# Kernel optimization log

Hardware: AMD Instinct MI355X
Metric: run time of the kernel (lower is better)

## Reference

```python
import jax, jax.numpy as jnp
import numpy as np

B, S, E = 2, 2048, 1024
H = 16
D = E // H  # head_dim = 64
SCALE = D ** -0.5


def _rope_cos_sin(seq_len, dim, dtype=jnp.float32):
    inv_freq = 1.0 / (10000.0 ** (jnp.arange(0, dim, 2, dtype=jnp.float32) / dim))
    pos = jnp.arange(seq_len, dtype=jnp.float32)
    freqs = pos[:, None] * inv_freq[None, :]  # [S, D/2]
    return jnp.cos(freqs).astype(dtype), jnp.sin(freqs).astype(dtype)


def _apply_rope(x, cos, sin):
    # x: [B, H, S, D]; interleaved complex rotation on (even, odd) pairs
    x2 = x.reshape(*x.shape[:-1], D // 2, 2)
    xr, xi = x2[..., 0], x2[..., 1]
    c = cos[None, None, :, :]
    s = sin[None, None, :, :]
    out_r = xr * c - xi * s
    out_i = xr * s + xi * c
    return jnp.stack([out_r, out_i], axis=-1).reshape(x.shape)


def setup_inputs() -> dict:
    key = jax.random.key(0)
    k1, k2, k3, k4, k5 = jax.random.split(key, 5)
    query = jax.random.normal(k1, (B, S, E), dtype=jnp.float32)
    key_t = jax.random.normal(k2, (B, S, E), dtype=jnp.float32)
    value = jax.random.normal(k3, (B, S, E), dtype=jnp.float32)
    w_qkv = jax.random.normal(k4, (3 * E, E), dtype=jnp.float32) * 0.02
    w_out = jax.random.normal(k5, (E, E), dtype=jnp.float32) * 0.02
    return {"query": query, "key": key_t, "value": value,
            "w_qkv": w_qkv, "w_out": w_out}


def reference(query, key, value, w_qkv, w_out):
    # Fused QKV projection from query only (matches original module)
    qkv = jnp.einsum('bse,fe->bsf', query, w_qkv)  # [B, S, 3E]
    q, k, v = jnp.split(qkv, 3, axis=-1)
    to_heads = lambda t: t.reshape(B, S, H, D).transpose(0, 2, 1, 3)  # [B,H,S,D]
    q, k, v = to_heads(q), to_heads(k), to_heads(v)

    cos, sin = _rope_cos_sin(S, D, q.dtype)
    q = _apply_rope(q, cos, sin)
    k = _apply_rope(k, cos, sin)

    # Standard scaled dot-product attention (eval mode, no mask, no dropout)
    attn = jnp.einsum('bhsd,bhtd->bhst', q, k) * SCALE
    attn = jax.nn.softmax(attn.astype(jnp.float32), axis=-1).astype(q.dtype)
    ctx = jnp.einsum('bhst,bhtd->bhsd', attn, v)  # [B,H,S,D]

    out = ctx.transpose(0, 2, 1, 3).reshape(B, S, E)
    return jnp.einsum('bse,fe->bsf', out, w_out)
```

## Files before the change

kernel.cpp:

```cpp
#include <hip/hip_runtime.h>
#include <math.h>

typedef __attribute__((ext_vector_type(8))) __bf16 bf16x8;
typedef __attribute__((ext_vector_type(4))) __bf16 bf16x4;
typedef __attribute__((ext_vector_type(4))) float f32x4;

constexpr int kBATCH = 2;
constexpr int kS = 2048;
constexpr int kE = 1024;
constexpr int kH = 16;
constexpr int kD = 64;
constexpr float kScale = 0.125f;
constexpr float kQScale = 0.125f * 1.44269504088896340736f;

__device__ inline void gl2lds16(const void* g, void* l) {
    __builtin_amdgcn_global_load_lds((const __attribute__((address_space(1))) void*)g,
                                     (__attribute__((address_space(3))) void*)l, 16, 0, 0);
}

__global__ __launch_bounds__(256) void cvt2_kernel(const float* __restrict__ a, __bf16* __restrict__ oa, int na,
                                                   const float* __restrict__ b, __bf16* __restrict__ ob,
                                                   float2* __restrict__ tab) {
    if (blockIdx.x >= 7168) {
        int e = (blockIdx.x - 7168) * 1024 + threadIdx.x * 4;
#pragma unroll
        for (int j = 0; j < 4; ++j) {
            int ee = e + j;
            int s = ee >> 5, i = ee & 31;
            float inv = expf(-(float)i * (9.210340371976184f / 32.0f));
            float ang = (float)s * inv;
            tab[ee] = make_float2(cosf(ang), sinf(ang));
        }
        return;
    }
    int idx = (blockIdx.x * 256 + threadIdx.x) * 4;
    const float* src;
    __bf16* dst;
    if (idx < na) { src = a + idx; dst = oa + idx; }
    else          { src = b + (idx - na); dst = ob + (idx - na); }
    float4 f = *(const float4*)src;
    bf16x4 r;
    r[0] = (__bf16)f.x; r[1] = (__bf16)f.y; r[2] = (__bf16)f.z; r[3] = (__bf16)f.w;
    *(bf16x4*)dst = r;
}

__global__ __launch_bounds__(256) void gemm_qkv_kernel(const __bf16* __restrict__ A,
                                                       const __bf16* __restrict__ W,
                                                       __bf16* __restrict__ vraw,
                                                       __bf16* __restrict__ qd,
                                                       __bf16* __restrict__ kd,
                                                       const float2* __restrict__ tab) {
    constexpr int kK = 1024;
    __shared__ __bf16 As[128 * 64] __attribute__((aligned(16)));
    __shared__ __bf16 Bs[128 * 64] __attribute__((aligned(16)));

    const int tid  = threadIdx.x;
    const int lane = tid & 63;
    const int quad = lane >> 4;
    const int l16  = lane & 15;
    const int rx   = l16 & 7;
    const int wave = tid >> 6;
    const int wm   = (wave >> 1) * 64;
    const int wn   = (wave & 1) * 64;
    const int m0   = blockIdx.y * 128;
    const int n0   = blockIdx.x * 128;

    const int srow8  = lane >> 3;
    const int schunk = ((lane & 7) ^ srow8) * 8;

    f32x4 zero = {0.f, 0.f, 0.f, 0.f};
    f32x4 acc[4][4];
#pragma unroll
    for (int i = 0; i < 4; ++i)
#pragma unroll
        for (int j = 0; j < 4; ++j) acc[i][j] = zero;

    for (int kt = 0; kt < kK; kt += 64) {
        __syncthreads();
#pragma unroll
        for (int i = 0; i < 4; ++i) {
            int rbase = wave * 32 + i * 8;
            gl2lds16(A + (size_t)(m0 + rbase + srow8) * kK + kt + schunk, &As[rbase * 64]);
            gl2lds16(W + (size_t)(n0 + rbase + srow8) * kK + kt + schunk, &Bs[rbase * 64]);
        }
        __syncthreads();

#pragma unroll
        for (int kk = 0; kk < 2; ++kk) {
            bf16x8 af[4], bf[4];
#pragma unroll
            for (int mi = 0; mi < 4; ++mi)
                af[mi] = *(const bf16x8*)(&As[(wm + mi * 16 + l16) * 64 + (((kk * 4 + quad) ^ rx)) * 8]);
#pragma unroll
            for (int ni = 0; ni < 4; ++ni)
                bf[ni] = *(const bf16x8*)(&Bs[(wn + ni * 16 + l16) * 64 + (((kk * 4 + quad) ^ rx)) * 8]);
#pragma unroll
            for (int mi = 0; mi < 4; ++mi)
#pragma unroll
                for (int ni = 0; ni < 4; ++ni)
                    acc[mi][ni] = __builtin_amdgcn_mfma_f32_16x16x32_bf16(af[mi], bf[ni], acc[mi][ni], 0, 0, 0);
        }
    }

    const int col0 = n0 + wn;
    const int reg  = col0 >> 10;
    const int h    = (col0 >> 6) & 15;

    if (reg == 2) {
#pragma unroll
        for (int mi = 0; mi < 4; ++mi)
#pragma unroll
            for (int ni = 0; ni < 4; ++ni)
#pragma unroll
                for (int r = 0; r < 4; ++r) {
                    int row  = m0 + wm + mi * 16 + quad * 4 + r;
                    int colv = col0 - 2048 + ni * 16 + l16;
                    vraw[(size_t)row * kE + colv] = (__bf16)acc[mi][ni][r];
                }
    } else {
        __bf16* dst = reg ? kd : qd;
        const float qs = reg ? 1.0f : kQScale;
        const bool odd = (l16 & 1);
#pragma unroll
        for (int mi = 0; mi < 4; ++mi)
#pragma unroll
            for (int r = 0; r < 4; ++r) {
                int srow = m0 + wm + mi * 16 + quad * 4 + r;
                int sloc = srow & (kS - 1);
                int bb   = srow >> 11;
                const float2* trow = tab + sloc * 32;
                __bf16* drow = dst + ((size_t)(bb * kH + h) * kS + sloc) * kD;
#pragma unroll
                for (int ni = 0; ni < 4; ++ni) {
                    int d = ni * 16 + l16;
                    float2 cs = trow[d >> 1];
                    float v  = acc[mi][ni][r];
                    float pv = __shfl_xor(v, 1);
                    float out = odd ? (pv * cs.y + v * cs.x) : (v * cs.x - pv * cs.y);
                    drow[d] = (__bf16)(qs * out);
                }
            }
    }
}

template <int TN, typename TC>
__global__ __launch_bounds__(256) void gemm_bt_kernel(const __bf16* __restrict__ A,
                                                      const __bf16* __restrict__ W,
                                                      TC* __restrict__ C,
                                                      int M, int N, int K) {
    constexpr int NI = TN / 32;
    __shared__ __bf16 As[128 * 64] __attribute__((aligned(16)));
    __shared__ __bf16 Bs[TN * 64] __attribute__((aligned(16)));

    const int tid  = threadIdx.x;
    const int lane = tid & 63;
    const int quad = lane >> 4;
    const int l16  = lane & 15;
    const int rx   = l16 & 7;
    const int wave = tid >> 6;
    const int wm   = (wave >> 1) * 64;
    const int wn   = (wave & 1) * (TN / 2);
    const int m0   = blockIdx.y * 128;
    const int n0   = blockIdx.x * TN;

    const int srow8  = lane >> 3;
    const int schunk = ((lane & 7) ^ srow8) * 8;

    f32x4 zero = {0.f, 0.f, 0.f, 0.f};
    f32x4 acc[4][NI];
#pragma unroll
    for (int i = 0; i < 4; ++i)
#pragma unroll
        for (int j = 0; j < NI; ++j) acc[i][j] = zero;

    for (int kt = 0; kt < K; kt += 64) {
        __syncthreads();
#pragma unroll
        for (int i = 0; i < 4; ++i) {
            int rbase = wave * 32 + i * 8;
            gl2lds16(A + (size_t)(m0 + rbase + srow8) * K + kt + schunk, &As[rbase * 64]);
        }
#pragma unroll
        for (int i = 0; i < NI; ++i) {
            int rbase = wave * (TN / 4) + i * 8;
            gl2lds16(W + (size_t)(n0 + rbase + srow8) * K + kt + schunk, &Bs[rbase * 64]);
        }
        __syncthreads();

#pragma unroll
        for (int kk = 0; kk < 2; ++kk) {
            bf16x8 af[4], bf[NI];
#pragma unroll
            for (int mi = 0; mi < 4; ++mi)
                af[mi] = *(const bf16x8*)(&As[(wm + mi * 16 + l16) * 64 + (((kk * 4 + quad) ^ rx)) * 8]);
#pragma unroll
            for (int ni = 0; ni < NI; ++ni)
                bf[ni] = *(const bf16x8*)(&Bs[(wn + ni * 16 + l16) * 64 + (((kk * 4 + quad) ^ rx)) * 8]);
#pragma unroll
            for (int mi = 0; mi < 4; ++mi)
#pragma unroll
                for (int ni = 0; ni < NI; ++ni)
                    acc[mi][ni] = __builtin_amdgcn_mfma_f32_16x16x32_bf16(af[mi], bf[ni], acc[mi][ni], 0, 0, 0);
        }
    }

#pragma unroll
    for (int mi = 0; mi < 4; ++mi)
#pragma unroll
        for (int ni = 0; ni < NI; ++ni)
#pragma unroll
            for (int r = 0; r < 4; ++r) {
                int row = m0 + wm + mi * 16 + quad * 4 + r;
                int col = n0 + wn + ni * 16 + l16;
                C[(size_t)row * N + col] = (TC)acc[mi][ni][r];
            }
}

__global__ __launch_bounds__(256) void vtrans_kernel(const __bf16* __restrict__ vraw,
                                                     __bf16* __restrict__ vt) {
    __shared__ __bf16 tile[64 * 72] __attribute__((aligned(16)));

    int flat = blockIdx.x;
    int s0 = (flat & 31) * 64;
    int bh = flat >> 5;
    int b = bh >> 4, h = bh & 15;
    int tid = threadIdx.x;

#pragma unroll
    for (int p = 0; p < 2; ++p) {
        int c = tid + p * 256;
        int r = c >> 3, jc = c & 7;
        *(bf16x8*)&tile[r * 72 + jc * 8] =
            *(const bf16x8*)(vraw + (size_t)(b * kS + s0 + r) * kE + h * kD + jc * 8);
    }
    __syncthreads();
#pragma unroll
    for (int p = 0; p < 2; ++p) {
        int c = tid + p * 256;
        int d = c >> 3, jt = c & 7;
        bf16x8 v;
#pragma unroll
        for (int u = 0; u < 8; ++u) {
            int src = (jt >> 2) * 32 + ((u >> 2) << 4) + ((jt & 3) << 2) + (u & 3);
            v[u] = tile[src * 72 + d];
        }
        *(bf16x8*)(vt + (size_t)(bh * kD + d) * kS + s0 + jt * 8) = v;
    }
}

__global__ __launch_bounds__(256, 2) void attn_kernel(const __bf16* __restrict__ qd,
                                                      const __bf16* __restrict__ kd,
                                                      const __bf16* __restrict__ vt,
                                                      __bf16* __restrict__ ctx,
                                                      const float* __restrict__ wout,
                                                      __bf16* __restrict__ woutb) {
    __shared__ __bf16 Ks[2][64 * 64] __attribute__((aligned(16)));
    __shared__ __bf16 Vs[4][64 * 64] __attribute__((aligned(16)));

    const int lane = threadIdx.x & 63;
    const int wave = threadIdx.x >> 6;
    const int quad = lane >> 4;
    const int l16  = lane & 15;
    const int rx   = l16 & 7;

    {
        int base = blockIdx.x * 2048 + threadIdx.x * 8;
#pragma unroll
        for (int p = 0; p < 2; ++p) {
            float4 f = *(const float4*)(wout + base + p * 4);
            bf16x4 r;
            r[0] = (__bf16)f.x; r[1] = (__bf16)f.y; r[2] = (__bf16)f.z; r[3] = (__bf16)f.w;
            *(bf16x4*)(woutb + base + p * 4) = r;
        }
    }

    const int flat = blockIdx.x;
    const int s    = flat >> 3;
    const int bh   = (flat & 7) * 4 + (s >> 4);
    const int q0   = (s & 15) * 128;
    const int b  = bh >> 4;
    const int h  = bh & 15;

    const __bf16* qp = qd + (size_t)bh * kS * kD;
    const __bf16* kp = kd + (size_t)bh * kS * kD;
    const __bf16* vp = vt + (size_t)bh * kD * kS;

    const int srow8  = lane >> 3;
    const int schunk = ((lane & 7) ^ srow8) * 8;

    bf16x8 aq[2][2];
#pragma unroll
    for (int qg = 0; qg < 2; ++qg) {
        const __bf16* qrow = qp + (size_t)(q0 + wave * 32 + qg * 16 + l16) * kD + quad * 8;
        aq[qg][0] = *(const bf16x8*)(qrow);
        aq[qg][1] = *(const bf16x8*)(qrow + 32);
    }

    bf16x8 vone;
#pragma unroll
    for (int u = 0; u < 8; ++u) vone[u] = (__bf16)1.0f;

    f32x4 zero = {0.f, 0.f, 0.f, 0.f};
    f32x4 acc[2][4];
    f32x4 asum[2] = {zero, zero};
#pragma unroll
    for (int qg = 0; qg < 2; ++qg)
#pragma unroll
        for (int i = 0; i < 4; ++i) acc[qg][i] = zero;

    f32x4 sgb[2][2][4];

    int koff[4][2], voff[4][2];
#pragma unroll
    for (int g = 0; g < 4; ++g) {
        int row = g * 16 + l16;
        koff[g][0] = row * 64 + ((quad       ^ rx)) * 8;
        koff[g][1] = row * 64 + (((quad + 4) ^ rx)) * 8;
        voff[g][0] = row * 64 + ((quad       ^ (row & 7))) * 8;
        voff[g][1] = row * 64 + (((quad + 4) ^ (row & 7))) * 8;
    }

    const __bf16* kst[2];
    const __bf16* vst[2];
#pragma unroll
    for (int c = 0; c < 2; ++c) {
        int i = wave * 2 + c;
        kst[c] = kp + (size_t)(i * 8 + srow8) * kD + schunk;
        vst[c] = vp + (size_t)(i * 8 + srow8) * kS + schunk;
    }

    auto stage = [&](int ks, int vs) __attribute__((always_inline)) -> void {
#pragma unroll
        for (int c = 0; c < 2; ++c) {
            gl2lds16(kst[c], &Ks[ks][(wave * 2 + c) * 512]);
            gl2lds16(vst[c], &Vs[vs][(wave * 2 + c) * 512]);
            kst[c] += 64 * kD;
            vst[c] += 64;
        }
    };

    auto qk = [&](int kbuf, int par) __attribute__((always_inline)) -> void {
#pragma unroll
        for (int g = 0; g < 4; ++g) {
            bf16x8 a0 = *(const bf16x8*)&Ks[kbuf][koff[g][0]];
            bf16x8 a1 = *(const bf16x8*)&Ks[kbuf][koff[g][1]];
#pragma unroll
            for (int qg = 0; qg < 2; ++qg) {
                f32x4 t = __builtin_amdgcn_mfma_f32_16x16x32_bf16(a0, aq[qg][0], zero, 0, 0, 0);
                sgb[par][qg][g] = __builtin_amdgcn_mfma_f32_16x16x32_bf16(a1, aq[qg][1], t, 0, 0, 0);
            }
        }
    };

    auto expand = [&](bf16x8 (&ap)[2][2], int par) __attribute__((always_inline)) -> void {
#pragma unroll
        for (int qg = 0; qg < 2; ++qg)
#pragma unroll
            for (int r = 0; r < 4; ++r) {
                ap[qg][0][r]     = (__bf16)__builtin_amdgcn_exp2f(sgb[par][qg][0][r]);
                ap[qg][0][4 + r] = (__bf16)__builtin_amdgcn_exp2f(sgb[par][qg][1][r]);
                ap[qg][1][r]     = (__bf16)__builtin_amdgcn_exp2f(sgb[par][qg][2][r]);
                ap[qg][1][4 + r] = (__bf16)__builtin_amdgcn_exp2f(sgb[par][qg][3][r]);
            }
    };

    auto sumpv = [&](int vbuf, bf16x8 (&ap)[2][2]) __attribute__((always_inline)) -> void {
#pragma unroll
        for (int qg = 0; qg < 2; ++qg) {
            asum[qg] = __builtin_amdgcn_mfma_f32_16x16x32_bf16(ap[qg][0], vone, asum[qg], 0, 0, 0);
            asum[qg] = __builtin_amdgcn_mfma_f32_16x16x32_bf16(ap[qg][1], vone, asum[qg], 0, 0, 0);
        }
#pragma unroll
        for (int nt = 0; nt < 4; ++nt) {
            bf16x8 bv0 = *(const bf16x8*)&Vs[vbuf][voff[nt][0]];
            bf16x8 bv1 = *(const bf16x8*)&Vs[vbuf][voff[nt][1]];
#pragma unroll
            for (int qg = 0; qg < 2; ++qg) {
                acc[qg][nt] = __builtin_amdgcn_mfma_f32_16x16x32_bf16(ap[qg][0], bv0, acc[qg][nt], 0, 0, 0);
                acc[qg][nt] = __builtin_amdgcn_mfma_f32_16x16x32_bf16(ap[qg][1], bv1, acc[qg][nt], 0, 0, 0);
            }
        }
    };

    auto body = [&](int kbuf, int vprev, int vnext, bool pf, int pin)
        __attribute__((always_inline)) -> void {
        __syncthreads();
        if (pf) stage(kbuf ^ 1, vnext);
        bf16x8 ap[2][2];
        expand(ap, pin);
        __builtin_amdgcn_s_setprio(1);
        qk(kbuf, pin ^ 1);
        sumpv(vprev, ap);
        __builtin_amdgcn_s_setprio(0);
    };

    stage(0, 0);
    __syncthreads();
    stage(1, 1);
    __builtin_amdgcn_s_setprio(1);
    qk(0, 0);
    __builtin_amdgcn_s_setprio(0);

#pragma unroll 1
    for (int t0 = 1; t0 < 29; t0 += 4) {
        body(1, 0, 2, true, 0);
        body(0, 1, 3, true, 1);
        body(1, 2, 0, true, 0);
        body(0, 3, 1, true, 1);
    }
    body(1, 0, 2, true, 0);
    body(0, 1, 3, true, 1);
    body(1, 2, 0, false, 0);

    {
        bf16x8 ap[2][2];
        expand(ap, 1);
        sumpv(3, ap);
    }

#pragma unroll
    for (int qg = 0; qg < 2; ++qg)
#pragma unroll
        for (int r = 0; r < 4; ++r) {
            float inv_l = 1.0f / asum[qg][r];
            int srow_q = q0 + wave * 32 + qg * 16 + quad * 4 + r;
#pragma unroll
            for (int nt = 0; nt < 4; ++nt) {
                int col = h * kD + nt * 16 + l16;
                ctx[(size_t)(b * kS + srow_q) * kE + col] = (__bf16)(acc[qg][nt][r] * inv_l);
            }
        }
}

extern "C" void kernel_launch(void* const* d_in, const int* in_sizes, int n_in,
                              void* d_out, int out_size, void* d_ws, size_t ws_size,
                              hipStream_t stream) {
    const float* query = (const float*)d_in[0];
    const float* w_qkv = (const float*)d_in[3];
    const float* w_out = (const float*)d_in[4];
    float* out = (float*)d_out;

    const int M = kBATCH * kS;
    const int nQ = M * kE;
    const int nWqkv = 3 * kE * kE;

    char* ws = (char*)d_ws;
    __bf16* query_b = (__bf16*)ws;
    __bf16* w_qkv_b = (__bf16*)(ws + ((size_t)8 << 20));
    float2* tab     = (float2*)(ws + ((size_t)14 << 20));
    __bf16* vraw    = (__bf16*)(ws + ((size_t)16 << 20));
    __bf16* qd      = (__bf16*)(ws + ((size_t)24 << 20));
    __bf16* kd      = (__bf16*)(ws + ((size_t)32 << 20));
    __bf16* vt      = (__bf16*)(ws + ((size_t)40 << 20));
    __bf16* ctx     = (__bf16*)ws;
    __bf16* w_out_b = (__bf16*)(ws + ((size_t)8 << 20));

    cvt2_kernel<<<7168 + 64, 256, 0, stream>>>(query, query_b, nQ, w_qkv, w_qkv_b, tab);

    gemm_qkv_kernel<<<dim3(3 * kE / 128, M / 128), 256, 0, stream>>>(
        query_b, w_qkv_b, vraw, qd, kd, tab);

    vtrans_kernel<<<1024, 256, 0, stream>>>(vraw, vt);

    attn_kernel<<<512, 256, 0, stream>>>(qd, kd, vt, ctx, w_out, w_out_b);

    gemm_bt_kernel<64, float>
        <<<dim3(kE / 64, M / 128), 256, 0, stream>>>(ctx, w_out_b, out, M, kE, kE);
}
```

Baseline: 202.3 us.

## Move RoPE out of QKV GEMM epilogue into separate K pass and attention Q load

The QKV GEMM epilogue no longer applies RoPE. It writes Q raw in head-major layout and K/V raw in row-major form. A combined rope_vtrans kernel rotates K into head-major layout and transposes V. The attention kernel applies RoPE and the softmax scale to Q when it loads it into registers. This is meant to remove the shuffle and table loads from the GEMM epilogue, at the cost of extra global traffic for K and a small per-block Q rotation. The workspace layout is also reshuffled, and kd now aliases the w_qkv_b buffer.

```diff
diff --git a/kernel.cpp b/kernel.cpp
--- a/kernel.cpp
+++ b/kernel.cpp
@@ -46,10 +46,8 @@
 
 __global__ __launch_bounds__(256) void gemm_qkv_kernel(const __bf16* __restrict__ A,
                                                        const __bf16* __restrict__ W,
-                                                       __bf16* __restrict__ vraw,
-                                                       __bf16* __restrict__ qd,
-                                                       __bf16* __restrict__ kd,
-                                                       const float2* __restrict__ tab) {
+                                                       __bf16* __restrict__ qkv_raw,
+                                                       __bf16* __restrict__ qd_raw) {
     constexpr int kK = 1024;
     __shared__ __bf16 As[128 * 64] __attribute__((aligned(16)));
     __shared__ __bf16 Bs[128 * 64] __attribute__((aligned(16)));
@@ -103,24 +101,8 @@
     }
 
     const int col0 = n0 + wn;
-    const int reg  = col0 >> 10;
-    const int h    = (col0 >> 6) & 15;
-
-    if (reg == 2) {
-#pragma unroll
-        for (int mi = 0; mi < 4; ++mi)
-#pragma unroll
-            for (int ni = 0; ni < 4; ++ni)
-#pragma unroll
-                for (int r = 0; r < 4; ++r) {
-                    int row  = m0 + wm + mi * 16 + quad * 4 + r;
-                    int colv = col0 - 2048 + ni * 16 + l16;
-                    vraw[(size_t)row * kE + colv] = (__bf16)acc[mi][ni][r];
-                }
-    } else {
-        __bf16* dst = reg ? kd : qd;
-        const float qs = reg ? 1.0f : kQScale;
-        const bool odd = (l16 & 1);
+    if (col0 < 1024) {
+        const int h = col0 >> 6;
 #pragma unroll
         for (int mi = 0; mi < 4; ++mi)
 #pragma unroll
@@ -128,18 +110,22 @@
                 int srow = m0 + wm + mi * 16 + quad * 4 + r;
                 int sloc = srow & (kS - 1);
                 int bb   = srow >> 11;
-                const float2* trow = tab + sloc * 32;
-                __bf16* drow = dst + ((size_t)(bb * kH + h) * kS + sloc) * kD;
-#pragma unroll
-                for (int ni = 0; ni < 4; ++ni) {
-                    int d = ni * 16 + l16;
-                    float2 cs = trow[d >> 1];
-                    float v  = acc[mi][ni][r];
-                    float pv = __shfl_xor(v, 1);
-                    float out = odd ? (pv * cs.y + v * cs.x) : (v * cs.x - pv * cs.y);
-                    drow[d] = (__bf16)(qs * out);
+                __bf16* drow = qd_raw + ((size_t)(bb * kH + h) * kS + sloc) * kD;
+#pragma unroll
+                for (int ni = 0; ni < 4; ++ni)
+                    drow[ni * 16 + l16] = (__bf16)acc[mi][ni][r];
+            }
+    } else {
+#pragma unroll
+        for (int mi = 0; mi < 4; ++mi)
+#pragma unroll
+            for (int ni = 0; ni < 4; ++ni)
+#pragma unroll
+                for (int r = 0; r < 4; ++r) {
+                    int row = m0 + wm + mi * 16 + quad * 4 + r;
+                    int col = col0 + ni * 16 + l16;
+                    qkv_raw[(size_t)row * (3 * kE) + col] = (__bf16)acc[mi][ni][r];
                 }
-            }
     }
 }
 
@@ -216,44 +202,72 @@
             }
 }
 
-__global__ __launch_bounds__(256) void vtrans_kernel(const __bf16* __restrict__ vraw,
-                                                     __bf16* __restrict__ vt) {
+__global__ __launch_bounds__(256) void rope_vtrans_kernel(const __bf16* __restrict__ qkv,
+                                                          __bf16* __restrict__ kd,
+                                                          __bf16* __restrict__ vt,
+                                                          const float2* __restrict__ tab) {
     __shared__ __bf16 tile[64 * 72] __attribute__((aligned(16)));
 
-    int flat = blockIdx.x;
-    int s0 = (flat & 31) * 64;
-    int bh = flat >> 5;
-    int b = bh >> 4, h = bh & 15;
-    int tid = threadIdx.x;
-
-#pragma unroll
-    for (int p = 0; p < 2; ++p) {
-        int c = tid + p * 256;
-        int r = c >> 3, jc = c & 7;
-        *(bf16x8*)&tile[r * 72 + jc * 8] =
-            *(const bf16x8*)(vraw + (size_t)(b * kS + s0 + r) * kE + h * kD + jc * 8);
-    }
-    __syncthreads();
-#pragma unroll
-    for (int p = 0; p < 2; ++p) {
-        int c = tid + p * 256;
-        int d = c >> 3, jt = c & 7;
-        bf16x8 v;
-#pragma unroll
-        for (int u = 0; u < 8; ++u) {
-            int src = (jt >> 2) * 32 + ((u >> 2) << 4) + ((jt & 3) << 2) + (u & 3);
-            v[u] = tile[src * 72 + d];
-        }
-        *(bf16x8*)(vt + (size_t)(bh * kD + d) * kS + s0 + jt * 8) = v;
-    }
-}
-
-__global__ __launch_bounds__(256, 2) void attn_kernel(const __bf16* __restrict__ qd,
+    if (blockIdx.x < 8192) {
+        int tid = blockIdx.x * 256 + threadIdx.x;
+        int i = tid & 31;
+        int h = (tid >> 5) & (kH - 1);
+        int s = (tid >> 9) & (kS - 1);
+        int b = tid >> 20;
+
+        size_t rowbase = (size_t)(b * kS + s) * (3 * kE);
+        int coff = h * kD + 2 * i;
+
+        union { uint u; __bf16 hx[2]; } ka, ko;
+        ka.u = *(const uint*)(qkv + rowbase + kE + coff);
+        float kr = (float)ka.hx[0];
+        float ki = (float)ka.hx[1];
+
+        float2 cs = tab[s * 32 + i];
+        float cv = cs.x;
+        float sv = cs.y;
+
+        size_t qbase = ((size_t)(b * kH + h) * kS + s) * kD + 2 * i;
+        ko.hx[0] = (__bf16)(kr * cv - ki * sv);
+        ko.hx[1] = (__bf16)(kr * sv + ki * cv);
+        *(uint*)(kd + qbase) = ko.u;
+    } else {
+        int flat = blockIdx.x - 8192;
+        int s0 = (flat & 31) * 64;
+        int bh = flat >> 5;
+        int b = bh >> 4, h = bh & 15;
+        int tid = threadIdx.x;
+
+#pragma unroll
+        for (int p = 0; p < 2; ++p) {
+            int c = tid + p * 256;
+            int r = c >> 3, jc = c & 7;
+            *(bf16x8*)&tile[r * 72 + jc * 8] =
+                *(const bf16x8*)(qkv + (size_t)(b * kS + s0 + r) * (3 * kE) + 2 * kE + h * kD + jc * 8);
+        }
+        __syncthreads();
+#pragma unroll
+        for (int p = 0; p < 2; ++p) {
+            int c = tid + p * 256;
+            int d = c >> 3, jt = c & 7;
+            bf16x8 v;
+#pragma unroll
+            for (int u = 0; u < 8; ++u) {
+                int src = (jt >> 2) * 32 + ((u >> 2) << 4) + ((jt & 3) << 2) + (u & 3);
+                v[u] = tile[src * 72 + d];
+            }
+            *(bf16x8*)(vt + (size_t)(bh * kD + d) * kS + s0 + jt * 8) = v;
+        }
+    }
+}
+
+__global__ __launch_bounds__(256, 2) void attn_kernel(const __bf16* __restrict__ qdr,
                                                       const __bf16* __restrict__ kd,
                                                       const __bf16* __restrict__ vt,
                                                       __bf16* __restrict__ ctx,
                                                       const float* __restrict__ wout,
-                                                      __bf16* __restrict__ woutb) {
+                                                      __bf16* __restrict__ woutb,
+                                                      const float2* __restrict__ tab) {
     __shared__ __bf16 Ks[2][64 * 64] __attribute__((aligned(16)));
     __shared__ __bf16 Vs[4][64 * 64] __attribute__((aligned(16)));
 
@@ -281,7 +295,7 @@
     const int b  = bh >> 4;
     const int h  = bh & 15;
 
-    const __bf16* qp = qd + (size_t)bh * kS * kD;
+    const __bf16* qp = qdr + (size_t)bh * kS * kD;
     const __bf16* kp = kd + (size_t)bh * kS * kD;
     const __bf16* vp = vt + (size_t)bh * kD * kS;
 
@@ -291,9 +305,30 @@
     bf16x8 aq[2][2];
 #pragma unroll
     for (int qg = 0; qg < 2; ++qg) {
-        const __bf16* qrow = qp + (size_t)(q0 + wave * 32 + qg * 16 + l16) * kD + quad * 8;
-        aq[qg][0] = *(const bf16x8*)(qrow);
-        aq[qg][1] = *(const bf16x8*)(qrow + 32);
+        int srowq = q0 + wave * 32 + qg * 16 + l16;
+        const __bf16* qrow = qp + (size_t)srowq * kD + quad * 8;
+        const float2* trow = tab + (size_t)srowq * 32;
+#pragma unroll
+        for (int fr = 0; fr < 2; ++fr) {
+            bf16x8 x = *(const bf16x8*)(qrow + fr * 32);
+            float4 csA = *(const float4*)(trow + quad * 4 + fr * 16);
+            float4 csB = *(const float4*)(trow + quad * 4 + fr * 16 + 2);
+            bf16x8 o;
+            float xr, xi;
+            xr = (float)x[0]; xi = (float)x[1];
+            o[0] = (__bf16)(kQScale * (xr * csA.x - xi * csA.y));
+            o[1] = (__bf16)(kQScale * (xr * csA.y + xi * csA.x));
+            xr = (float)x[2]; xi = (float)x[3];
+            o[2] = (__bf16)(kQScale * (xr * csA.z - xi * csA.w));
+            o[3] = (__bf16)(kQScale * (xr * csA.w + xi * csA.z));
+            xr = (float)x[4]; xi = (float)x[5];
+            o[4] = (__bf16)(kQScale * (xr * csB.x - xi * csB.y));
+            o[5] = (__bf16)(kQScale * (xr * csB.y + xi * csB.x));
+            xr = (float)x[6]; xi = (float)x[7];
+            o[6] = (__bf16)(kQScale * (xr * csB.z - xi * csB.w));
+            o[7] = (__bf16)(kQScale * (xr * csB.w + xi * csB.z));
+            aq[qg][fr] = o;
+        }
     }
 
     bf16x8 vone;
@@ -445,24 +480,24 @@
     const int nWqkv = 3 * kE * kE;
 
     char* ws = (char*)d_ws;
-    __bf16* query_b = (__bf16*)ws;
-    __bf16* w_qkv_b = (__bf16*)(ws + ((size_t)8 << 20));
-    float2* tab     = (float2*)(ws + ((size_t)14 << 20));
-    __bf16* vraw    = (__bf16*)(ws + ((size_t)16 << 20));
-    __bf16* qd      = (__bf16*)(ws + ((size_t)24 << 20));
-    __bf16* kd      = (__bf16*)(ws + ((size_t)32 << 20));
-    __bf16* vt      = (__bf16*)(ws + ((size_t)40 << 20));
+    __bf16* qkv_raw = (__bf16*)ws;
     __bf16* ctx     = (__bf16*)ws;
-    __bf16* w_out_b = (__bf16*)(ws + ((size_t)8 << 20));
+    __bf16* w_out_b = (__bf16*)(ws + (size_t)8388608);
+    __bf16* query_b = (__bf16*)(ws + (size_t)25165824);
+    __bf16* w_qkv_b = (__bf16*)(ws + (size_t)33554432);
+    __bf16* kd      = w_qkv_b;
+    __bf16* vt      = (__bf16*)(ws + (size_t)41943040);
+    float2* tab     = (float2*)(ws + ((size_t)48 << 20));
+    __bf16* qd_raw  = (__bf16*)(ws + ((size_t)52 << 20));
 
     cvt2_kernel<<<7168 + 64, 256, 0, stream>>>(query, query_b, nQ, w_qkv, w_qkv_b, tab);
 
     gemm_qkv_kernel<<<dim3(3 * kE / 128, M / 128), 256, 0, stream>>>(
-        query_b, w_qkv_b, vraw, qd, kd, tab);
-
-    vtrans_kernel<<<1024, 256, 0, stream>>>(vraw, vt);
-
-    attn_kernel<<<512, 256, 0, stream>>>(qd, kd, vt, ctx, w_out, w_out_b);
+        query_b, w_qkv_b, qkv_raw, qd_raw);
+
+    rope_vtrans_kernel<<<8192 + 1024, 256, 0, stream>>>(qkv_raw, kd, vt, tab);
+
+    attn_kernel<<<512, 256, 0, stream>>>(qd_raw, kd, vt, ctx, w_out, w_out_b, tab);
 
     gemm_bt_kernel<64, float>
         <<<dim3(kE / 64, M / 128), 256, 0, stream>>>(ctx, w_out_b, out, M, kE, kE);
```

Result: no change. 203.1 us (+0.4%).
